# Kernel optimization log

Hardware: AMD Instinct MI355X
Metric: run time of the kernel (lower is better)

## Reference

```python
import jax, jax.numpy as jnp
import numpy as np

V = 50000; H = 600; HH = 300; L = 100; MAX_LEN = 50; T_IN = 48; T_TGT = 50; EOS = 1


def setup_inputs() -> dict:
    key = jax.random.key(0)
    ks = iter(jax.random.split(key, 40))
    def p(shape, s=0.05):
        return jax.random.normal(next(ks), shape, dtype=jnp.float32) * s
    inp = {}
    inp["emb_enc"] = p((V, H)); inp["emb_dec"] = p((V, H))
    for pre in ["enc", "dec"]:
        for d in ["f", "b"]:
            inp[pre + "_wih_" + d] = p((3 * HH, H))
            inp[pre + "_whh_" + d] = p((3 * HH, HH))
            inp[pre + "_bih_" + d] = p((3 * HH,))
            inp[pre + "_bhh_" + d] = p((3 * HH,))
    inp["w_mean"] = p((L, H)); inp["b_mean"] = p((L,))
    inp["w_logv"] = p((L, H)); inp["b_logv"] = p((L,))
    inp["w_l2h"] = p((H, L)); inp["b_l2h"] = p((H,))
    inp["attn_w"] = p((MAX_LEN, 2 * H)); inp["attn_b"] = p((MAX_LEN,))
    inp["comb_w"] = p((H, 2 * H)); inp["comb_b"] = p((H,))
    inp["out_w"] = p((V, H)); inp["out_b"] = p((V,))
    inp["eps"] = jax.random.normal(next(ks), (MAX_LEN, L), dtype=jnp.float32)
    inp["input_tokens"] = jax.random.randint(next(ks), (T_IN,), 0, V)
    inp["target_tokens"] = jax.random.randint(next(ks), (T_TGT,), 0, V)
    return inp


def _gru_cell(x, h, wih, whh, bih, bhh):
    # PyTorch GRUCell math: r,z,n gates
    gi = wih @ x + bih
    gh = whh @ h + bhh
    ir, iz, inn = jnp.split(gi, 3)
    hr, hz, hn = jnp.split(gh, 3)
    r = jax.nn.sigmoid(ir + hr)
    zg = jax.nn.sigmoid(iz + hz)
    n = jnp.tanh(inn + r * hn)
    return (1.0 - zg) * n + zg * h


def _forward(emb_enc, emb_dec,
             enc_wih_f, enc_whh_f, enc_bih_f, enc_bhh_f,
             enc_wih_b, enc_whh_b, enc_bih_b, enc_bhh_b,
             dec_wih_f, dec_whh_f, dec_bih_f, dec_bhh_f,
             dec_wih_b, dec_whh_b, dec_bih_b, dec_bhh_b,
             w_mean, b_mean, w_logv, b_logv, w_l2h, b_l2h,
             attn_w, attn_b, comb_w, comb_b, out_w, out_b,
             eps, input_tokens, target_tokens):
    # --- encoder: bidirectional GRU fed one token at a time (both dirs see the
    # same forward stream since the original calls the GRU with seq_len=1) ---
    def enc_step(carry, tok):
        hf, hb = carry
        x = emb_enc[tok]
        hf2 = _gru_cell(x, hf, enc_wih_f, enc_whh_f, enc_bih_f, enc_bhh_f)
        hb2 = _gru_cell(x, hb, enc_wih_b, enc_whh_b, enc_bih_b, enc_bhh_b)
        return (hf2, hb2), jnp.concatenate([hf2, hb2])
    h0 = jnp.zeros((HH,), dtype=emb_enc.dtype)
    (hf, hb), enc_out = jax.lax.scan(enc_step, (h0, h0), input_tokens)
    enc_outputs = jnp.zeros((MAX_LEN, H), dtype=emb_enc.dtype).at[:input_tokens.shape[0]].set(enc_out)
    # --- latent ---
    mean = enc_outputs @ w_mean.T + b_mean          # (MAX_LEN, L)
    logv = enc_outputs @ w_logv.T + b_logv          # (MAX_LEN, L)
    z = eps * jnp.exp(0.5 * logv) + mean
    latent_out = z @ w_l2h.T + b_l2h                # (MAX_LEN, H)
    # --- decoder with attention over latent_out (teacher forcing) ---
    dec_in = jnp.concatenate([jnp.array([EOS], dtype=target_tokens.dtype), target_tokens[:-1]])
    def dec_step(carry, tok):
        hf, hb = carry
        emb = emb_dec[tok]                          # (H,) dropout==identity (eval)
        hflat = jnp.concatenate([hf, hb])           # (H,)
        aw = jax.nn.softmax(attn_w @ jnp.concatenate([emb, hflat]) + attn_b)  # (MAX_LEN,)
        applied = aw @ latent_out                   # (H,)
        o = jax.nn.relu(comb_w @ jnp.concatenate([emb, applied]) + comb_b)
        hf2 = _gru_cell(o, hf, dec_wih_f, dec_whh_f, dec_bih_f, dec_bhh_f)
        hb2 = _gru_cell(o, hb, dec_wih_b, dec_whh_b, dec_bih_b, dec_bhh_b)
        logp = jax.nn.log_softmax(out_w @ jnp.concatenate([hf2, hb2]) + out_b)
        return (hf2, hb2), logp
    _, decoded = jax.lax.scan(dec_step, (hf, hb), dec_in)  # (T_TGT, V)
    return decoded, mean, logv


def reference(emb_enc, emb_dec,
              enc_wih_f, enc_whh_f, enc_bih_f, enc_bhh_f,
              enc_wih_b, enc_whh_b, enc_bih_b, enc_bhh_b,
              dec_wih_f, dec_whh_f, dec_bih_f, dec_bhh_f,
              dec_wih_b, dec_whh_b, dec_bih_b, dec_bhh_b,
              w_mean, b_mean, w_logv, b_logv, w_l2h, b_l2h,
              attn_w, attn_b, comb_w, comb_b, out_w, out_b,
              eps, input_tokens, target_tokens):
    return _forward(emb_enc, emb_dec,
                    enc_wih_f, enc_whh_f, enc_bih_f, enc_bhh_f,
                    enc_wih_b, enc_whh_b, enc_bih_b, enc_bhh_b,
                    dec_wih_f, dec_whh_f, dec_bih_f, dec_bhh_f,
                    dec_wih_b, dec_whh_b, dec_bih_b, dec_bhh_b,
                    w_mean, b_mean, w_logv, b_logv, w_l2h, b_l2h,
                    attn_w, attn_b, comb_w, comb_b, out_w, out_b,
                    eps, input_tokens, target_tokens)
```

## Files before the change

### kernel.cpp

```cpp
#include <hip/hip_runtime.h>
#include <math.h>

#define VSZ 50000
#define HD 600
#define HHD 300
#define LATD 100
#define MLEN 50
#define TIN 48
#define TTGT 50
#define NBLK 75
#define NTHR 512
#define NTOT (NBLK*NTHR)
#define ESTR 640
#define SLOT_STRIDE 32
#define SENTU 0x40000000u

typedef __attribute__((ext_vector_type(4))) float f32x4;
typedef __attribute__((ext_vector_type(8))) short s16x8;

__device__ __forceinline__ float sigf(float x){ return 1.0f/(1.0f+__expf(-x)); }

__device__ __forceinline__ void stf(float* p, float v){
    __hip_atomic_store((unsigned int*)p, __float_as_uint(v),
                       __ATOMIC_RELAXED, __HIP_MEMORY_SCOPE_AGENT);
}
__device__ __forceinline__ void stu(float* p, unsigned v){
    __hip_atomic_store((unsigned int*)p, v,
                       __ATOMIC_RELAXED, __HIP_MEMORY_SCOPE_AGENT);
}
__device__ __forceinline__ int ldslot(const int* p){
    return __hip_atomic_load(p, __ATOMIC_RELAXED, __HIP_MEMORY_SCOPE_AGENT);
}
__device__ __forceinline__ void stslot(int* p, int v){
    __hip_atomic_store(p, v, __ATOMIC_RELAXED, __HIP_MEMORY_SCOPE_AGENT);
}

__device__ __forceinline__ f32x4 ld_unc16(const float* p){
    f32x4 r;
    asm volatile("global_load_dwordx4 %0, %1, off sc0 sc1\n\ts_waitcnt vmcnt(0)"
                 : "=v"(r) : "v"(p) : "memory");
    return r;
}
__device__ __forceinline__ f32x4 poll16(const float* p){
    f32x4 r = ld_unc16(p);
    while (__float_as_uint(r[0])==SENTU || __float_as_uint(r[1])==SENTU ||
           __float_as_uint(r[2])==SENTU || __float_as_uint(r[3])==SENTU){
        __builtin_amdgcn_s_sleep(1);
        r = ld_unc16(p);
    }
    return r;
}

__device__ __forceinline__ void redu3(float&a,float&b,float&c){
    #pragma unroll
    for(int off=32;off;off>>=1){
        a+=__shfl_xor(a,off); b+=__shfl_xor(b,off); c+=__shfl_xor(c,off);
    }
}
__device__ __forceinline__ void redu6(float&a,float&b,float&c,float&d,float&e,float&f){
    #pragma unroll
    for(int off=32;off;off>>=1){
        a+=__shfl_xor(a,off); b+=__shfl_xor(b,off); c+=__shfl_xor(c,off);
        d+=__shfl_xor(d,off); e+=__shfl_xor(e,off); f+=__shfl_xor(f,off);
    }
}

__device__ __forceinline__ void gridbar(int* slots, int* flags, int e){
    asm volatile("s_waitcnt vmcnt(0)" ::: "memory");
    __syncthreads();
    const int tid = threadIdx.x;
    if (tid == 0) stslot(&slots[blockIdx.x*SLOT_STRIDE], e);
    if (blockIdx.x == 0){
        if (tid < NBLK){
            while (ldslot(&slots[tid*SLOT_STRIDE]) < e)
                __builtin_amdgcn_s_sleep(1);
        }
        __syncthreads();
        if (tid < NBLK) stslot(&flags[tid*SLOT_STRIDE], e);
    } else {
        if (tid == 0){
            while (ldslot(&flags[blockIdx.x*SLOT_STRIDE]) < e)
                __builtin_amdgcn_s_sleep(1);
        }
    }
    __syncthreads();
}

__global__ void k_init(int* sync_mem){
    int i = blockIdx.x*blockDim.x + threadIdx.x;
    if (i < 2*NBLK*SLOT_STRIDE) sync_mem[i] = 0;
}

__global__ void __launch_bounds__(NTHR, 2) k_seq(
    const float* __restrict__ emb_enc, const float* __restrict__ emb_dec,
    const float* __restrict__ enc_wih_f, const float* __restrict__ enc_whh_f,
    const float* __restrict__ enc_bih_f, const float* __restrict__ enc_bhh_f,
    const float* __restrict__ enc_wih_b, const float* __restrict__ enc_whh_b,
    const float* __restrict__ enc_bih_b, const float* __restrict__ enc_bhh_b,
    const float* __restrict__ dec_wih_f, const float* __restrict__ dec_whh_f,
    const float* __restrict__ dec_bih_f, const float* __restrict__ dec_bhh_f,
    const float* __restrict__ dec_wih_b, const float* __restrict__ dec_whh_b,
    const float* __restrict__ dec_bih_b, const float* __restrict__ dec_bhh_b,
    const float* __restrict__ w_mean, const float* __restrict__ b_mean,
    const float* __restrict__ w_logv, const float* __restrict__ b_logv,
    const float* __restrict__ w_l2h, const float* __restrict__ b_l2h,
    const float* __restrict__ attn_w, const float* __restrict__ attn_b,
    const float* __restrict__ comb_w, const float* __restrict__ comb_b,
    const float* __restrict__ eps, const int* __restrict__ in_toks,
    const int* __restrict__ tgt_toks,
    float* __restrict__ GIf, float* __restrict__ ENCf,
    float* __restrict__ Zf, float* __restrict__ LATf, float* __restrict__ Mf,
    float* __restrict__ APREf, float* __restrict__ CPREf,
    float* __restrict__ HSs, float* __restrict__ HSv,
    float* __restrict__ out_mean, float* __restrict__ out_logv,
    int* slots, int* flags){

    __shared__ float h_lds[ESTR];
    __shared__ float o_lds[ESTR];
    __shared__ float s_lds[64];
    __shared__ float aw_lds[64];
    __shared__ float hv_lds[8];
    __shared__ float big_lds[HD*MLEN];

    const int tid  = threadIdx.x;
    const int lane = tid & 63;
    const int wid  = tid >> 6;
    const int gtid = blockIdx.x*NTHR + tid;
    const int gw   = blockIdx.x*8 + wid;
    const int dir  = gw / HHD;
    const int k    = gw % HHD;
    int ep = 0;

    const int dlo = (blockIdx.x*8) / HHD, dhi = (blockIdx.x*8 + 7) / HHD;
    const int clo = (dlo==dhi) ? dlo*75 : 0;
    const int chi = (dlo==dhi) ? clo+75 : 150;
    const int flo = 4*clo, fhi = 4*chi;

    for (int j=tid; j<ESTR; j+=NTHR){ h_lds[j]=0.f; o_lds[j]=0.f; }

    for (int idx=gtid; idx<TIN*HD; idx+=NTOT){
        int t=idx/HD, j=idx%HD;
        stu(&ENCf[(long)t*ESTR + j], SENTU);
    }
    for (int idx=gtid; idx<TTGT*HD; idx+=NTOT){
        int t=idx/HD, j=idx%HD;
        stu(&HSs[(long)t*ESTR + j], SENTU);
    }
    for (int idx=gtid; idx<TIN*1800; idx+=NTOT){
        int t=idx/1800, r=idx%1800, d=r/900, j=r%900;
        const float* w  = d ? enc_wih_b : enc_wih_f;
        const float* bi = d ? enc_bih_b : enc_bih_f;
        const float* x  = emb_enc + (long)in_toks[t]*HD;
        const float* wr = w + (long)j*HD;
        float acc = bi[j];
        for (int kk=0;kk<HD;kk+=4){
            float4 wv = *(const float4*)(wr+kk);
            float4 xv = *(const float4*)(x+kk);
            acc = fmaf(wv.x,xv.x,acc); acc = fmaf(wv.y,xv.y,acc);
            acc = fmaf(wv.z,xv.z,acc); acc = fmaf(wv.w,xv.w,acc);
        }
        stf(&GIf[idx], acc);
    }
    for (int idx=gtid; idx<TTGT*MLEN; idx+=NTOT){
        int t=idx/MLEN, a=idx%MLEN;
        int tok = t ? tgt_toks[t-1] : 1;
        const float* x  = emb_dec + (long)tok*HD;
        const float* wr = attn_w + (long)a*1200;
        float acc = attn_b[a];
        for (int kk=0;kk<HD;kk+=4){
            float4 wv = *(const float4*)(wr+kk);
            float4 xv = *(const float4*)(x+kk);
            acc = fmaf(wv.x,xv.x,acc); acc = fmaf(wv.y,xv.y,acc);
            acc = fmaf(wv.z,xv.z,acc); acc = fmaf(wv.w,xv.w,acc);
        }
        stf(&APREf[idx], acc);
    }
    for (int idx=gtid; idx<TTGT*HD; idx+=NTOT){
        int t=idx/HD, j=idx%HD;
        int tok = t ? tgt_toks[t-1] : 1;
        const float* x  = emb_dec + (long)tok*HD;
        const float* wr = comb_w + (long)j*1200;
        float acc = comb_b[j];
        for (int kk=0;kk<HD;kk+=4){
            float4 wv = *(const float4*)(wr+kk);
            float4 xv = *(const float4*)(x+kk);
            acc = fmaf(wv.x,xv.x,acc); acc = fmaf(wv.y,xv.y,acc);
            acc = fmaf(wv.z,xv.z,acc); acc = fmaf(wv.w,xv.w,acc);
        }
        stf(&CPREf[idx], acc);
    }
    gridbar(slots, flags, ++ep);

    {
        const float* whh = dir ? enc_whh_b : enc_whh_f;
        const float* bhh = dir ? enc_bhh_b : enc_bhh_f;
        float wr_[5], wz_[5], wn_[5];
        #pragma unroll
        for (int i=0;i<5;i++){
            int k2 = lane + 64*i;
            bool ok = k2 < HHD;
            wr_[i] = ok ? whh[(long)k*HHD + k2] : 0.f;
            wz_[i] = ok ? whh[(long)(HHD+k)*HHD + k2] : 0.f;
            wn_[i] = ok ? whh[(long)(2*HHD+k)*HHD + k2] : 0.f;
        }
        const float bhr = bhh[k], bhz = bhh[HHD+k], bhn = bhh[2*HHD+k];
        float gr=0, gz=0, gn=0;
        if (lane < TIN){
            const float* g = GIf + (long)lane*1800 + dir*900;
            gr = g[k]; gz = g[HHD+k]; gn = g[2*HHD+k];
        }
        for (int t=0; t<TIN; t++){
            if (t){
                if (tid < chi-clo)
                    *(f32x4*)&h_lds[4*(clo+tid)] = poll16(&ENCf[(long)(t-1)*ESTR + 4*(clo+tid)]);
            }
            __syncthreads();
            if (t){
                for (int j=flo+tid; j<fhi; j+=NTHR)
                    big_lds[(long)(t-1)*HD + j] = h_lds[j];
            }
            float sr=0, sz=0, sn=0;
            #pragma unroll
            for (int i=0;i<5;i++){
                float hv = h_lds[dir*HHD + lane + 64*i];
                sr = fmaf(wr_[i], hv, sr);
                sz = fmaf(wz_[i], hv, sz);
                sn = fmaf(wn_[i], hv, sn);
            }
            redu3(sr, sz, sn);
            float grt=__shfl(gr,t), gzt=__shfl(gz,t), gnt=__shfl(gn,t);
            if (lane==0){
                float r = sigf(grt + sr + bhr);
                float z = sigf(gzt + sz + bhz);
                float n = tanhf(gnt + r*(sn + bhn));
                float hp = h_lds[gw];
                hv_lds[wid] = (1.f-z)*n + z*hp;
            }
            __syncthreads();
            if (tid < 8) stf(&ENCf[(long)t*ESTR + blockIdx.x*8 + tid], hv_lds[tid]);
        }
        if (tid < HD/4)
            *(f32x4*)&h_lds[4*tid] = poll16(&ENCf[(long)(TIN-1)*ESTR + 4*tid]);
        __syncthreads();
        big_lds[(long)(TIN-1)*HD + tid] = h_lds[tid];
        if (tid < HD-NTHR) big_lds[(long)(TIN-1)*HD + NTHR + tid] = h_lds[NTHR+tid];
        big_lds[(long)TIN*HD + tid] = 0.f;
        big_lds[(long)TIN*HD + NTHR + tid] = 0.f;
        if (tid < 2*HD - 2*NTHR) big_lds[(long)TIN*HD + 2*NTHR + tid] = 0.f;
        {
            int compn = 150 - (chi - clo);
            for (int q=tid; q<47*compn; q+=NTHR){
                int row = q / compn, c = q % compn;
                int ch = (c < clo) ? c : (c + (chi - clo));
                *(f32x4*)&big_lds[(long)row*HD + 4*ch] =
                    poll16(&ENCf[(long)row*ESTR + 4*ch]);
            }
        }
        __syncthreads();
    }

    for (int idx=gtid; idx<MLEN*LATD; idx+=NTOT){
        int i=idx/LATD, l=idx%LATD;
        const float* e = &big_lds[(long)i*HD];
        const float* wmr = w_mean + (long)l*HD;
        float am = b_mean[l];
        for (int kk=0;kk<HD;kk+=4){
            f32x4 wv = *(const f32x4*)(wmr+kk);
            f32x4 ev = *(const f32x4*)(e+kk);
            am = fmaf(wv[0],ev[0],am); am = fmaf(wv[1],ev[1],am);
            am = fmaf(wv[2],ev[2],am); am = fmaf(wv[3],ev[3],am);
        }
        const float* wlr = w_logv + (long)l*HD;
        float al = b_logv[l];
        for (int kk=0;kk<HD;kk+=4){
            f32x4 wv = *(const f32x4*)(wlr+kk);
            f32x4 ev = *(const f32x4*)(e+kk);
            al = fmaf(wv[0],ev[0],al); al = fmaf(wv[1],ev[1],al);
            al = fmaf(wv[2],ev[2],al); al = fmaf(wv[3],ev[3],al);
        }
        out_mean[idx] = am;
        out_logv[idx] = al;
        stf(&Zf[idx], eps[idx]*__expf(0.5f*al) + am);
    }
    gridbar(slots, flags, ++ep);
    for (int idx=gtid; idx<MLEN*HD; idx+=NTOT){
        int i=idx/HD, j=idx%HD;
        const float* zr = Zf + (long)i*LATD;
        const float* wr = w_l2h + (long)j*LATD;
        float acc = b_l2h[j];
        for (int kk=0;kk<LATD;kk+=4){
            float4 wv = *(const float4*)(wr+kk);
            float4 zv = *(const float4*)(zr+kk);
            acc = fmaf(wv.x,zv.x,acc); acc = fmaf(wv.y,zv.y,acc);
            acc = fmaf(wv.z,zv.z,acc); acc = fmaf(wv.w,zv.w,acc);
        }
        stf(&LATf[idx], acc);
    }
    gridbar(slots, flags, ++ep);
    for (int idx=gtid; idx<MLEN*HD; idx+=NTOT){
        int j=idx/MLEN, i=idx%MLEN;
        const float* wr = comb_w + (long)j*1200 + HD;
        const float* lr = LATf + (long)i*HD;
        float acc = 0.f;
        for (int kk=0;kk<HD;kk+=4){
            float4 wv = *(const float4*)(wr+kk);
            float4 lv = *(const float4*)(lr+kk);
            acc = fmaf(wv.x,lv.x,acc); acc = fmaf(wv.y,lv.y,acc);
            acc = fmaf(wv.z,lv.z,acc); acc = fmaf(wv.w,lv.w,acc);
        }
        stf(&Mf[idx], acc);
    }
    gridbar(slots, flags, ++ep);

    {
        for (int idx=tid; idx<HD*MLEN/4; idx+=NTHR)
            *(f32x4*)&big_lds[4*idx] = *(const f32x4*)&Mf[4*idx];

        float awr[7][10];
        #pragma unroll
        for (int ai=0; ai<7; ai++){
            int a = wid + 8*ai;
            #pragma unroll
            for (int i=0;i<10;i++){
                int kk = lane + 64*i;
                awr[ai][i] = (a < MLEN && kk < HD) ? attn_w[(long)a*1200 + HD + kk] : 0.f;
            }
        }

        const float* wih = dir ? dec_wih_b : dec_wih_f;
        const float* bih = dir ? dec_bih_b : dec_bih_f;
        const float* whh = dir ? dec_whh_b : dec_whh_f;
        const float* bhh = dir ? dec_bhh_b : dec_bhh_f;
        float ur[10], uz[10], un[10];
        #pragma unroll
        for (int i=0;i<10;i++){
            int k2 = lane + 64*i;
            bool ok = k2 < HD;
            ur[i] = ok ? wih[(long)k*HD + k2] : 0.f;
            uz[i] = ok ? wih[(long)(HHD+k)*HD + k2] : 0.f;
            un[i] = ok ? wih[(long)(2*HHD+k)*HD + k2] : 0.f;
        }
        float vr[5], vz[5], vn[5];
        #pragma unroll
        for (int i=0;i<5;i++){
            int k2 = lane + 64*i;
            bool ok = k2 < HHD;
            vr[i] = ok ? whh[(long)k*HHD + k2] : 0.f;
            vz[i] = ok ? whh[(long)(HHD+k)*HHD + k2] : 0.f;
            vn[i] = ok ? whh[(long)(2*HHD+k)*HHD + k2] : 0.f;
        }
        const float bir = bih[k], biz = bih[HHD+k], bin_ = bih[2*HHD+k];
        const float bhr = bhh[k], bhz = bhh[HHD+k], bhn = bhh[2*HHD+k];

        for (int t=0; t<TTGT; t++){
            if (t){
                if (tid < HD/4)
                    *(f32x4*)&h_lds[4*tid] = poll16(&HSs[(long)(t-1)*ESTR + 4*tid]);
            }
            float cp0 = CPREf[(long)t*HD + tid];
            float cp1 = (tid < HD-NTHR) ? CPREf[(long)t*HD + NTHR + tid] : 0.f;
            __syncthreads();
            #pragma unroll
            for (int ai=0; ai<7; ai++){
                int a = wid + 8*ai;
                if (a < MLEN){
                    float acc = 0.f;
                    #pragma unroll
                    for (int i=0;i<10;i++)
                        acc = fmaf(awr[ai][i], h_lds[lane + 64*i], acc);
                    #pragma unroll
                    for (int off=32;off;off>>=1) acc += __shfl_xor(acc,off);
                    if (lane==0) s_lds[a] = acc + APREf[t*MLEN + a];
                }
            }
            __syncthreads();
            if (wid==0){
                float v = (lane<MLEN) ? s_lds[lane] : -1e30f;
                float m = v;
                #pragma unroll
                for (int off=32;off;off>>=1) m = fmaxf(m, __shfl_xor(m,off));
                float e = (lane<MLEN) ? __expf(v-m) : 0.f;
                float sum = 0.f;
                #pragma unroll
                for (int a=0;a<MLEN;a++) sum += __shfl(e, a);
                float inv = 1.f/sum;
                if (lane<MLEN) aw_lds[lane] = e*inv;
            }
            __syncthreads();
            for (int j=tid; j<HD; j+=NTHR){
                float acc = (j==tid) ? cp0 : cp1;
                const float* mr = &big_lds[j*MLEN];
                #pragma unroll
                for (int i=0;i<MLEN;i++) acc = fmaf(mr[i], aw_lds[i], acc);
                o_lds[j] = fmaxf(acc, 0.f);
            }
            __syncthreads();
            float ar=0,az=0,an=0, hr=0,hz=0,hn=0;
            #pragma unroll
            for (int i=0;i<10;i++){
                float ov = o_lds[lane + 64*i];
                ar = fmaf(ur[i], ov, ar);
                az = fmaf(uz[i], ov, az);
                an = fmaf(un[i], ov, an);
            }
            #pragma unroll
            for (int i=0;i<5;i++){
                float hv = h_lds[dir*HHD + lane + 64*i];
                hr = fmaf(vr[i], hv, hr);
                hz = fmaf(vz[i], hv, hz);
                hn = fmaf(vn[i], hv, hn);
            }
            redu6(ar,az,an,hr,hz,hn);
            if (lane==0){
                float r = sigf(ar + bir + hr + bhr);
                float zg = sigf(az + biz + hz + bhz);
                float n = tanhf(an + bin_ + r*(hn + bhn));
                hv_lds[wid] = (1.f-zg)*n + zg*h_lds[gw];
            }
            __syncthreads();
            if (tid < 8){
                float hnew = hv_lds[tid];
                stf(&HSs[(long)t*ESTR + blockIdx.x*8 + tid], hnew);
                HSv[(long)t*HD + blockIdx.x*8 + tid] = hnew;
            }
        }
    }
}

__device__ __forceinline__ s16x8 pack8(const float* __restrict__ p){
    s16x8 r;
    #pragma unroll
    for (int i=0;i<8;i++){
        unsigned u = __float_as_uint(p[i]);
        r[i] = (short)((u + 0x7fffu + ((u>>16)&1u)) >> 16);
    }
    return r;
}

__global__ void __launch_bounds__(256) k_vocab(const float* __restrict__ out_w,
        const float* __restrict__ out_b, const float* __restrict__ HS,
        float* __restrict__ logits){
    int lane = threadIdx.x & 63, wid = threadIdx.x >> 6;
    int vbase = blockIdx.x*64 + wid*16;
    int arow  = vbase + (lane & 15);
    int kg    = (lane >> 4) * 8;
    bool aok  = arow < VSZ;
    const float* ap = out_w + (long)(aok ? arow : 0) * HD;
    int t0 = lane & 15;
    f32x4 acc0 = {0,0,0,0}, acc1 = acc0, acc2 = acc0, acc3 = acc0;
    const s16x8 zf = (s16x8)0;

    for (int ks=0; ks<19; ks++){
        int kb = ks*32 + kg;
        bool kok = kb < HD;
        s16x8 a = (aok && kok) ? pack8(ap + kb) : zf;
        s16x8 b0 = kok              ? pack8(HS + (long)(t0     )*HD + kb) : zf;
        s16x8 b1 = kok              ? pack8(HS + (long)(t0 + 16)*HD + kb) : zf;
        s16x8 b2 = kok              ? pack8(HS + (long)(t0 + 32)*HD + kb) : zf;
        s16x8 b3 = (kok && t0 < 2)  ? pack8(HS + (long)(t0 + 48)*HD + kb) : zf;
        acc0 = __builtin_amdgcn_mfma_f32_16x16x32_bf16(a, b0, acc0, 0,0,0);
        acc1 = __builtin_amdgcn_mfma_f32_16x16x32_bf16(a, b1, acc1, 0,0,0);
        acc2 = __builtin_amdgcn_mfma_f32_16x16x32_bf16(a, b2, acc2, 0,0,0);
        acc3 = __builtin_amdgcn_mfma_f32_16x16x32_bf16(a, b3, acc3, 0,0,0);
    }

    int vst = vbase + (lane>>4)*4;
    float bb[4];
    #pragma unroll
    for (int r=0;r<4;r++) bb[r] = (vst+r < VSZ) ? out_b[vst+r] : 0.f;
    #pragma unroll
    for (int f=0; f<4; f++){
        int t = t0 + 16*f;
        if (t >= TTGT) continue;
        const f32x4 acc = f==0?acc0 : f==1?acc1 : f==2?acc2 : acc3;
        float* rowp = logits + (long)t*VSZ;
        #pragma unroll
        for (int r=0;r<4;r++){
            int v = vst + r;
            if (v < VSZ) rowp[v] = acc[r] + bb[r];
        }
    }
}

__global__ void __launch_bounds__(1024) k_lsm(float* __restrict__ logits){
    __shared__ float red[16];
    __shared__ float sm, sl;
    long t = blockIdx.x;
    float* row = logits + t*VSZ;
    int tid = threadIdx.x, lane = tid&63, w = tid>>6;
    float m = -1e30f;
    for (int v=tid; v<VSZ; v+=1024) m = fmaxf(m, row[v]);
    #pragma unroll
    for (int off=32;off;off>>=1) m = fmaxf(m, __shfl_xor(m,off));
    if (lane==0) red[w] = m;
    __syncthreads();
    if (tid==0){ float mm=red[0]; for (int i=1;i<16;i++) mm=fmaxf(mm,red[i]); sm=mm; }
    __syncthreads();
    float mx = sm;
    float s = 0.f;
    for (int v=tid; v<VSZ; v+=1024) s += __expf(row[v]-mx);
    #pragma unroll
    for (int off=32;off;off>>=1) s += __shfl_xor(s,off);
    __syncthreads();
    if (lane==0) red[w] = s;
    __syncthreads();
    if (tid==0){ float ss=0.f; for (int i=0;i<16;i++) ss+=red[i]; sl = logf(ss); }
    __syncthreads();
    float lg = sl;
    for (int v=tid; v<VSZ; v+=1024) row[v] = row[v] - mx - lg;
}

extern "C" void kernel_launch(void* const* d_in, const int* in_sizes, int n_in,
                              void* d_out, int out_size, void* d_ws, size_t ws_size,
                              hipStream_t stream) {
    const float* emb_enc   = (const float*)d_in[0];
    const float* emb_dec   = (const float*)d_in[1];
    const float* enc_wih_f = (const float*)d_in[2];
    const float* enc_whh_f = (const float*)d_in[3];
    const float* enc_bih_f = (const float*)d_in[4];
    const float* enc_bhh_f = (const float*)d_in[5];
    const float* enc_wih_b = (const float*)d_in[6];
    const float* enc_whh_b = (const float*)d_in[7];
    const float* enc_bih_b = (const float*)d_in[8];
    const float* enc_bhh_b = (const float*)d_in[9];
    const float* dec_wih_f = (const float*)d_in[10];
    const float* dec_whh_f = (const float*)d_in[11];
    const float* dec_bih_f = (const float*)d_in[12];
    const float* dec_bhh_f = (const float*)d_in[13];
    const float* dec_wih_b = (const float*)d_in[14];
    const float* dec_whh_b = (const float*)d_in[15];
    const float* dec_bih_b = (const float*)d_in[16];
    const float* dec_bhh_b = (const float*)d_in[17];
    const float* w_mean    = (const float*)d_in[18];
    const float* b_mean    = (const float*)d_in[19];
    const float* w_logv    = (const float*)d_in[20];
    const float* b_logv    = (const float*)d_in[21];
    const float* w_l2h     = (const float*)d_in[22];
    const float* b_l2h     = (const float*)d_in[23];
    const float* attn_w    = (const float*)d_in[24];
    const float* attn_b    = (const float*)d_in[25];
    const float* comb_w    = (const float*)d_in[26];
    const float* comb_b    = (const float*)d_in[27];
    const float* out_w     = (const float*)d_in[28];
    const float* out_b     = (const float*)d_in[29];
    const float* eps       = (const float*)d_in[30];
    const int*   in_toks   = (const int*)d_in[31];
    const int*   tgt_toks  = (const int*)d_in[32];

    float* ws = (float*)d_ws;
    float* GIf   = ws;
    float* ENCf  = ws + 86400;
    float* Zf    = ws + 118400;
    float* LATf  = ws + 123424;
    float* Mf    = ws + 153440;
    float* APREf = ws + 183456;
    float* CPREf = ws + 185984;
    float* HSs   = ws + 216000;
    float* HSv   = ws + 248000;
    int*   slots = (int*)(ws + 278016);
    int*   flags = (int*)(ws + 280416);

    float* dec_out  = (float*)d_out;
    float* out_mean = dec_out + 2500000;
    float* out_logv = dec_out + 2505000;

    k_init<<<(2*NBLK*SLOT_STRIDE + 255)/256, 256, 0, stream>>>((int*)(ws + 278016));

    k_seq<<<NBLK, NTHR, 0, stream>>>(
        emb_enc, emb_dec,
        enc_wih_f, enc_whh_f, enc_bih_f, enc_bhh_f,
        enc_wih_b, enc_whh_b, enc_bih_b, enc_bhh_b,
        dec_wih_f, dec_whh_f, dec_bih_f, dec_bhh_f,
        dec_wih_b, dec_whh_b, dec_bih_b, dec_bhh_b,
        w_mean, b_mean, w_logv, b_logv, w_l2h, b_l2h,
        attn_w, attn_b, comb_w, comb_b,
        eps, in_toks, tgt_toks,
        GIf, ENCf, Zf, LATf, Mf, APREf, CPREf, HSs, HSv,
        out_mean, out_logv, slots, flags);

    k_vocab<<<(VSZ + 63)/64, 256, 0, stream>>>(out_w, out_b, HSv, dec_out);
    k_lsm<<<TTGT, 1024, 0, stream>>>(dec_out);
}
```

Before: 782.0 us.

## Split log-softmax into chunked two-pass kernels and drop per-step LDS staging

```diff
diff --git a/kernel.cpp b/kernel.cpp
--- a/kernel.cpp
+++ b/kernel.cpp
@@ -119,7 +119,6 @@
     __shared__ float o_lds[ESTR];
     __shared__ float s_lds[64];
     __shared__ float aw_lds[64];
-    __shared__ float hv_lds[8];
     __shared__ float big_lds[HD*MLEN];
 
     const int tid  = threadIdx.x;
@@ -234,10 +233,9 @@
                 float z = sigf(gzt + sz + bhz);
                 float n = tanhf(gnt + r*(sn + bhn));
                 float hp = h_lds[gw];
-                hv_lds[wid] = (1.f-z)*n + z*hp;
-            }
-            __syncthreads();
-            if (tid < 8) stf(&ENCf[(long)t*ESTR + blockIdx.x*8 + tid], hv_lds[tid]);
+                stf(&ENCf[(long)t*ESTR + gw], (1.f-z)*n + z*hp);
+            }
+            __syncthreads();
         }
         if (tid < HD/4)
             *(f32x4*)&h_lds[4*tid] = poll16(&ENCf[(long)(TIN-1)*ESTR + 4*tid]);
@@ -415,14 +413,11 @@
                 float r = sigf(ar + bir + hr + bhr);
                 float zg = sigf(az + biz + hz + bhz);
                 float n = tanhf(an + bin_ + r*(hn + bhn));
-                hv_lds[wid] = (1.f-zg)*n + zg*h_lds[gw];
-            }
-            __syncthreads();
-            if (tid < 8){
-                float hnew = hv_lds[tid];
-                stf(&HSs[(long)t*ESTR + blockIdx.x*8 + tid], hnew);
-                HSv[(long)t*HD + blockIdx.x*8 + tid] = hnew;
-            }
+                float hnew = (1.f-zg)*n + zg*h_lds[gw];
+                stf(&HSs[(long)t*ESTR + gw], hnew);
+                HSv[(long)t*HD + gw] = hnew;
+            }
+            __syncthreads();
         }
     }
 }
@@ -482,32 +477,45 @@
     }
 }
 
-__global__ void __launch_bounds__(1024) k_lsm(float* __restrict__ logits){
-    __shared__ float red[16];
-    __shared__ float sm, sl;
-    long t = blockIdx.x;
-    float* row = logits + t*VSZ;
+#define LCH 12500
+
+__global__ void __launch_bounds__(256) k_lsm1(const float* __restrict__ logits,
+                                              float* __restrict__ part){
+    __shared__ float red[8];
+    int row = blockIdx.x >> 2, c = blockIdx.x & 3;
+    const float* x = logits + (long)row*VSZ + c*LCH;
     int tid = threadIdx.x, lane = tid&63, w = tid>>6;
     float m = -1e30f;
-    for (int v=tid; v<VSZ; v+=1024) m = fmaxf(m, row[v]);
+    for (int v=tid; v<LCH; v+=256) m = fmaxf(m, x[v]);
     #pragma unroll
     for (int off=32;off;off>>=1) m = fmaxf(m, __shfl_xor(m,off));
     if (lane==0) red[w] = m;
     __syncthreads();
-    if (tid==0){ float mm=red[0]; for (int i=1;i<16;i++) mm=fmaxf(mm,red[i]); sm=mm; }
+    float mm = fmaxf(fmaxf(red[0],red[1]),fmaxf(red[2],red[3]));
+    float s = 0.f;
+    for (int v=tid; v<LCH; v+=256) s += __expf(x[v]-mm);
+    #pragma unroll
+    for (int off=32;off;off>>=1) s += __shfl_xor(s,off);
+    if (lane==0) red[4+w] = s;
     __syncthreads();
-    float mx = sm;
-    float s = 0.f;
-    for (int v=tid; v<VSZ; v+=1024) s += __expf(row[v]-mx);
-    #pragma unroll
-    for (int off=32;off;off>>=1) s += __shfl_xor(s,off);
-    __syncthreads();
-    if (lane==0) red[w] = s;
-    __syncthreads();
-    if (tid==0){ float ss=0.f; for (int i=0;i<16;i++) ss+=red[i]; sl = logf(ss); }
-    __syncthreads();
-    float lg = sl;
-    for (int v=tid; v<VSZ; v+=1024) row[v] = row[v] - mx - lg;
+    if (tid==0){
+        part[(row*4+c)*2+0] = mm;
+        part[(row*4+c)*2+1] = red[4]+red[5]+red[6]+red[7];
+    }
+}
+
+__global__ void __launch_bounds__(256) k_lsm2(float* __restrict__ logits,
+                                              const float* __restrict__ part){
+    int row = blockIdx.x >> 2, c = blockIdx.x & 3;
+    const float* pr = part + row*8;
+    float M = fmaxf(fmaxf(pr[0],pr[2]),fmaxf(pr[4],pr[6]));
+    float S = pr[1]*__expf(pr[0]-M);
+    S += pr[3]*__expf(pr[2]-M);
+    S += pr[5]*__expf(pr[4]-M);
+    S += pr[7]*__expf(pr[6]-M);
+    float L = logf(S);
+    float* x = logits + (long)row*VSZ + c*LCH;
+    for (int v=threadIdx.x; v<LCH; v+=256) x[v] = x[v] - M - L;
 }
 
 extern "C" void kernel_launch(void* const* d_in, const int* in_sizes, int n_in,
@@ -559,6 +567,7 @@
     float* HSv   = ws + 248000;
     int*   slots = (int*)(ws + 278016);
     int*   flags = (int*)(ws + 280416);
+    float* PART  = ws + 282816;
 
     float* dec_out  = (float*)d_out;
     float* out_mean = dec_out + 2500000;
@@ -579,5 +588,6 @@
         out_mean, out_logv, slots, flags);
 
     k_vocab<<<(VSZ + 63)/64, 256, 0, stream>>>(out_w, out_b, HSv, dec_out);
-    k_lsm<<<TTGT, 1024, 0, stream>>>(dec_out);
-}
+    k_lsm1<<<200, 256, 0, stream>>>(dec_out, PART);
+    k_lsm2<<<200, 256, 0, stream>>>(dec_out, PART);
+}
```

New measurement: 848.2 us. +8.5%, slower.
